# Performance work log

Hardware: AMD Instinct MI355X
Metric: run time of the kernel (lower is better)

The kernel has to match this reference:

```python
import jax, jax.numpy as jnp
import numpy as np

EPS = 1e-5

def setup_inputs() -> dict:
    key = jax.random.key(0)
    k1, k2, k3, k4, k5 = jax.random.split(key, 5)
    N, E, D = 50000, 1600000, 128
    feat = jax.random.normal(k1, (N, D), dtype=jnp.float32)
    edge_index = jax.random.randint(k2, (2, E), 0, N, dtype=jnp.int64)
    W = jax.random.normal(k3, (D, D), dtype=jnp.float32) * (1.0 / np.sqrt(D))
    b = jax.random.normal(k4, (D,), dtype=jnp.float32) * 0.01
    gamma = jnp.ones((D,), dtype=jnp.float32)
    beta = jnp.zeros((D,), dtype=jnp.float32)
    return {"feat": feat, "edge_index": edge_index, "W": W, "b": b, "gamma": gamma, "beta": beta}

def reference(feat, edge_index, W, b, gamma, beta):
    # feat: [N, D] node features; edge_index: [2, E] (src, dst)
    N = feat.shape[0]
    src, dst = edge_index[0], edge_index[1]
    ones = jnp.ones(src.shape, dtype=feat.dtype)
    # out-degree of source nodes, in-degree of destination nodes
    deg_out = jnp.clip(jax.ops.segment_sum(ones, src, num_segments=N), 1.0)
    deg_in = jnp.clip(jax.ops.segment_sum(ones, dst, num_segments=N), 1.0)
    # pre-scale by D_out^{-1/2}, aggregate messages (copy_src + sum)
    feat_src = feat * jax.lax.rsqrt(deg_out)[:, None]        # [N, D]
    agg = jax.ops.segment_sum(feat_src[src], dst, num_segments=N)  # [N, D]
    # linear projection then post-scale by D_in^{-1/2}
    rst = agg @ W.T + b
    rst = rst * jax.lax.rsqrt(deg_in)[:, None]
    # identity residual (in_dim == out_dim)
    rst = rst + feat
    # LayerNorm(out_dim)
    mu = jnp.mean(rst, axis=-1, keepdims=True)
    var = jnp.var(rst, axis=-1, keepdims=True)
    rst = (rst - mu) * jax.lax.rsqrt(var + EPS) * gamma + beta
    # relu activation
    return jax.nn.relu(rst)
```

## Files before the change

kernel.cpp:

```cpp
#include <hip/hip_runtime.h>
#include <hip/hip_fp16.h>

#define LN_EPS 1e-5f
#define D 128
#define TN 16
#define BCAP 768
#define MAXB 4096
#define BBLK 256
#define HBLK 2048
#define NREP 8
#define AGG_LD 136

typedef _Float16 f16x4 __attribute__((ext_vector_type(4)));
typedef float f32x4 __attribute__((ext_vector_type(4)));

__global__ __launch_bounds__(256) void k_build(const int* __restrict__ ei, int E,
        int* __restrict__ cnt_out, int* __restrict__ bcnt,
        unsigned int* __restrict__ bkt, int NB, int Np) {
    __shared__ int h[MAXB];
    __shared__ int cur[MAXB];
    int tid = threadIdx.x;
    int E4 = E >> 2;
    const int4* src4 = (const int4*)ei;
    const int4* dst4 = (const int4*)(ei + E);

    if (blockIdx.x >= BBLK) {
        int* co = cnt_out + (size_t)(blockIdx.x & (NREP - 1)) * Np;
        int gtid = (blockIdx.x - BBLK) * 256 + tid;
        int gstride = (gridDim.x - BBLK) * 256;
        for (int i = gtid; i < E4; i += gstride) {
            int4 s = src4[i];
            atomicAdd(&co[s.x], 1);
            atomicAdd(&co[s.y], 1);
            atomicAdd(&co[s.z], 1);
            atomicAdd(&co[s.w], 1);
        }
        for (int e = (E4 << 2) + gtid; e < E; e += gstride) {
            atomicAdd(&co[ei[e]], 1);
        }
        return;
    }

    int chunk4 = (E4 + BBLK - 1) / BBLK;
    int lo4 = blockIdx.x * chunk4;
    int hi4 = min(E4, lo4 + chunk4);
    bool last = (blockIdx.x == BBLK - 1);

    for (int k = tid; k < NB; k += 256) h[k] = 0;
    __syncthreads();

    for (int i = lo4 + tid; i < hi4; i += 256) {
        int4 d = dst4[i];
        atomicAdd(&h[d.x >> 4], 1);
        atomicAdd(&h[d.y >> 4], 1);
        atomicAdd(&h[d.z >> 4], 1);
        atomicAdd(&h[d.w >> 4], 1);
    }
    if (last) {
        for (int e = (E4 << 2) + tid; e < E; e += 256)
            atomicAdd(&h[ei[E + e] >> 4], 1);
    }
    __syncthreads();

    for (int k = tid; k < NB; k += 256) {
        int c = h[k];
        cur[k] = c ? atomicAdd(&bcnt[k], c) : 0;
    }
    __syncthreads();

    for (int i = lo4 + tid; i < hi4; i += 256) {
        int4 s = src4[i];
        int4 d = dst4[i];
        int p0 = atomicAdd(&cur[d.x >> 4], 1);
        int p1 = atomicAdd(&cur[d.y >> 4], 1);
        int p2 = atomicAdd(&cur[d.z >> 4], 1);
        int p3 = atomicAdd(&cur[d.w >> 4], 1);
        if (p0 < BCAP) bkt[(size_t)(d.x >> 4) * BCAP + p0] = (unsigned)s.x | ((unsigned)(d.x & 15) << 16);
        if (p1 < BCAP) bkt[(size_t)(d.y >> 4) * BCAP + p1] = (unsigned)s.y | ((unsigned)(d.y & 15) << 16);
        if (p2 < BCAP) bkt[(size_t)(d.z >> 4) * BCAP + p2] = (unsigned)s.z | ((unsigned)(d.z & 15) << 16);
        if (p3 < BCAP) bkt[(size_t)(d.w >> 4) * BCAP + p3] = (unsigned)s.w | ((unsigned)(d.w & 15) << 16);
    }
    if (last) {
        for (int e = (E4 << 2) + tid; e < E; e += 256) {
            int s = ei[e], dd = ei[E + e];
            int p = atomicAdd(&cur[dd >> 4], 1);
            if (p < BCAP) bkt[(size_t)(dd >> 4) * BCAP + p] = (unsigned)s | ((unsigned)(dd & 15) << 16);
        }
    }
}

__global__ __launch_bounds__(256) void k_rs(const int* __restrict__ cnt_out,
                                            float* __restrict__ rs_out,
                                            const float* __restrict__ W,
                                            __half2* __restrict__ Wh2, int N, int Np) {
    int i = blockIdx.x * blockDim.x + threadIdx.x;
    if (i < N) {
        int so = 0;
        #pragma unroll
        for (int r = 0; r < NREP; ++r) so += cnt_out[(size_t)r * Np + i];
        rs_out[i] = rsqrtf((float)max(so, 1));
    }
    if (i < D * D / 2) {
        float2 w2 = ((const float2*)W)[i];
        Wh2[i] = __floats2half2_rn(w2.x, w2.y);
    }
}

__global__ __launch_bounds__(256) void k_prep(const float4* __restrict__ feat4,
                                              const float* __restrict__ rs_out,
                                              ushort4* __restrict__ feat_h,
                                              int total ) {
    int stride = gridDim.x * blockDim.x;
    for (int i = blockIdx.x * blockDim.x + threadIdx.x; i < total; i += stride) {
        int n = i >> 5;
        float rs = rs_out[n];
        float4 f = feat4[i];
        __half2 lo = __floats2half2_rn(f.x * rs, f.y * rs);
        __half2 hi = __floats2half2_rn(f.z * rs, f.w * rs);
        ushort4 u;
        u.x = __half_as_ushort(__low2half(lo));
        u.y = __half_as_ushort(__high2half(lo));
        u.z = __half_as_ushort(__low2half(hi));
        u.w = __half_as_ushort(__high2half(hi));
        feat_h[i] = u;
    }
}

__global__ __launch_bounds__(512) void k_fused(
        const int* __restrict__ bcnt, const unsigned int* __restrict__ bkt,
        const uint4* __restrict__ fh16, const _Float16* __restrict__ Wh,
        const float* __restrict__ bias, const float* __restrict__ gamma,
        const float* __restrict__ beta, const float* __restrict__ feat,
        float* __restrict__ out, int N) {
    __shared__ _Float16 aggH[TN * AGG_LD];
    __shared__ float redS[8][TN];
    __shared__ float redQ[8][TN];
    __shared__ unsigned short blist[BCAP];
    __shared__ int bstart[TN + 1];
    __shared__ int bfill[TN];
    __shared__ int bdeg[TN];

    int tid  = threadIdx.x;
    int wv   = tid >> 6;
    int lane = tid & 63;
    int l15  = lane & 15;
    int lg   = lane >> 4;

    int dA = wv * 16 + l15;
    float bd0 = bias[dA];
    float gd0 = gamma[dA];
    float bt0 = beta[dA];

    f16x4 Bf[8];
    #pragma unroll
    for (int kb = 0; kb < 8; ++kb)
        Bf[kb] = *reinterpret_cast<const f16x4*>(&Wh[(size_t)dA * D + kb * 16 + lg * 4]);

    int ntiles = (N + TN - 1) / TN;

    int t = blockIdx.x;
    unsigned v0c = 0, v1c = 0;
    int ec_c = 0;
    if (t < ntiles) {
        ec_c = min(bcnt[t], BCAP);
        v0c = bkt[(size_t)t * BCAP + tid];
        v1c = (tid + 512 < BCAP) ? bkt[(size_t)t * BCAP + tid + 512] : 0u;
    }

    for (; t < ntiles; t += gridDim.x) {
        int t2 = t + gridDim.x;
        unsigned v0n = 0, v1n = 0;
        int ec_n = 0;
        if (t2 < ntiles) {
            ec_n = min(bcnt[t2], BCAP);
            v0n = bkt[(size_t)t2 * BCAP + tid];
            v1n = (tid + 512 < BCAP) ? bkt[(size_t)t2 * BCAP + tid + 512] : 0u;
        }

        int nbase = t * TN;
        __syncthreads();
        if (tid < TN) { bdeg[tid] = 0; bfill[tid] = 0; }
        __syncthreads();

        if (tid < ec_c)       atomicAdd(&bdeg[v0c >> 16], 1);
        if (tid + 512 < ec_c) atomicAdd(&bdeg[v1c >> 16], 1);
        __syncthreads();

        if (tid < 16) {
            int v = bdeg[tid];
            int inc = v;
            #pragma unroll
            for (int off = 1; off < 16; off <<= 1) {
                int u = __shfl_up(inc, off, 16);
                if (tid >= off) inc += u;
            }
            bstart[tid] = inc - v;
            if (tid == 15) bstart[16] = inc;
        }
        __syncthreads();

        if (tid < ec_c) {
            int node = v0c >> 16;
            int slot = bstart[node] + atomicAdd(&bfill[node], 1);
            blist[slot] = (unsigned short)(v0c & 0xFFFF);
        }
        if (tid + 512 < ec_c) {
            int node = v1c >> 16;
            int slot = bstart[node] + atomicAdd(&bfill[node], 1);
            blist[slot] = (unsigned short)(v1c & 0xFFFF);
        }
        __syncthreads();

        {
            int row  = wv * 2 + (lg & 1);
            int half = lg >> 1;
            int n    = nbase + row;
            float va[8];
            #pragma unroll
            for (int k = 0; k < 8; ++k) va[k] = 0.0f;
            if (n < N) {
                int deg = bdeg[row];
                int st  = bstart[row];
                int cnt = (deg > half) ? ((deg - half + 1) >> 1) : 0;
                int base = st + half;
                int j = 0;
                for (; j + 8 <= cnt; j += 8) {
                    int ss[8];
                    #pragma unroll
                    for (int k = 0; k < 8; ++k) ss[k] = blist[base + 2 * (j + k)];
                    uint4 vv[8];
                    #pragma unroll
                    for (int k = 0; k < 8; ++k) vv[k] = fh16[(size_t)ss[k] * 16 + l15];
                    #pragma unroll
                    for (int k = 0; k < 8; ++k) {
                        float2 f;
                        f = __half22float2(__builtin_bit_cast(__half2, vv[k].x));
                        va[0] += f.x; va[1] += f.y;
                        f = __half22float2(__builtin_bit_cast(__half2, vv[k].y));
                        va[2] += f.x; va[3] += f.y;
                        f = __half22float2(__builtin_bit_cast(__half2, vv[k].z));
                        va[4] += f.x; va[5] += f.y;
                        f = __half22float2(__builtin_bit_cast(__half2, vv[k].w));
                        va[6] += f.x; va[7] += f.y;
                    }
                }
                for (; j < cnt; ++j) {
                    int s = blist[base + 2 * j];
                    uint4 vv = fh16[(size_t)s * 16 + l15];
                    float2 f;
                    f = __half22float2(__builtin_bit_cast(__half2, vv.x)); va[0] += f.x; va[1] += f.y;
                    f = __half22float2(__builtin_bit_cast(__half2, vv.y)); va[2] += f.x; va[3] += f.y;
                    f = __half22float2(__builtin_bit_cast(__half2, vv.z)); va[4] += f.x; va[5] += f.y;
                    f = __half22float2(__builtin_bit_cast(__half2, vv.w)); va[6] += f.x; va[7] += f.y;
                }
            }
            #pragma unroll
            for (int k = 0; k < 8; ++k) va[k] += __shfl_xor(va[k], 32);
            if (half == 0) {
                __half2 h0 = __floats2half2_rn(va[0], va[1]);
                __half2 h1 = __floats2half2_rn(va[2], va[3]);
                __half2 h2 = __floats2half2_rn(va[4], va[5]);
                __half2 h3 = __floats2half2_rn(va[6], va[7]);
                uint4 o;
                o.x = __builtin_bit_cast(unsigned int, h0);
                o.y = __builtin_bit_cast(unsigned int, h1);
                o.z = __builtin_bit_cast(unsigned int, h2);
                o.w = __builtin_bit_cast(unsigned int, h3);
                *reinterpret_cast<uint4*>(&aggH[row * AGG_LD + l15 * 8]) = o;
            }
        }
        __syncthreads();

        f32x4 acc = {0.0f, 0.0f, 0.0f, 0.0f};
        #pragma unroll
        for (int kb = 0; kb < 8; ++kb) {
            f16x4 a = *reinterpret_cast<const f16x4*>(&aggH[l15 * AGG_LD + kb * 16 + lg * 4]);
            acc = __builtin_amdgcn_mfma_f32_16x16x16f16(a, Bf[kb], acc, 0, 0, 0);
        }

        float rv[4];
        #pragma unroll
        for (int r = 0; r < 4; ++r) {
            int m = lg * 4 + r;
            int n = nbase + m;
            float f0 = 0.0f;
            if (n < N) {
                float rsin = rsqrtf((float)max(bdeg[m], 1));
                f0 = (acc[r] + bd0) * rsin + feat[(size_t)n * D + dA];
            }
            rv[r] = f0;
            float s = f0;
            float q = f0 * f0;
            s += __shfl_xor(s, 1);  q += __shfl_xor(q, 1);
            s += __shfl_xor(s, 2);  q += __shfl_xor(q, 2);
            s += __shfl_xor(s, 4);  q += __shfl_xor(q, 4);
            s += __shfl_xor(s, 8);  q += __shfl_xor(q, 8);
            if (l15 == 0) { redS[wv][m] = s; redQ[wv][m] = q; }
        }
        __syncthreads();

        #pragma unroll
        for (int r = 0; r < 4; ++r) {
            int m = lg * 4 + r;
            int n = nbase + m;
            if (n < N) {
                float S = redS[0][m] + redS[1][m] + redS[2][m] + redS[3][m]
                        + redS[4][m] + redS[5][m] + redS[6][m] + redS[7][m];
                float Q = redQ[0][m] + redQ[1][m] + redQ[2][m] + redQ[3][m]
                        + redQ[4][m] + redQ[5][m] + redQ[6][m] + redQ[7][m];
                float mu  = S * (1.0f / 128.0f);
                float var = Q * (1.0f / 128.0f) - mu * mu;
                float inv = rsqrtf(var + LN_EPS);
                float v0 = (rv[r] - mu) * inv * gd0 + bt0;
                out[(size_t)n * D + dA] = fmaxf(v0, 0.0f);
            }
        }

        v0c = v0n; v1c = v1n; ec_c = ec_n;
    }
}

extern "C" void kernel_launch(void* const* d_in, const int* in_sizes, int n_in,
                              void* d_out, int out_size, void* d_ws, size_t ws_size,
                              hipStream_t stream) {
    const float* feat  = (const float*)d_in[0];
    const int*   ei    = (const int*)  d_in[1];
    const float* W     = (const float*)d_in[2];
    const float* bias  = (const float*)d_in[3];
    const float* gamma = (const float*)d_in[4];
    const float* beta  = (const float*)d_in[5];
    float* out = (float*)d_out;

    const int N  = in_sizes[0] / D;
    const int E  = in_sizes[1] / 2;
    const int NB = (N + TN - 1) / TN;

    const size_t Np  = ((size_t)N + 1023) & ~(size_t)1023;
    const size_t NBp = ((size_t)NB + 1023) & ~(size_t)1023;
    int*   cnt_out = (int*)d_ws;
    int*   bcnt    = cnt_out + NREP * Np;
    float* rs_out  = (float*)(bcnt + NBp);
    _Float16* Wh   = (_Float16*)(rs_out + Np);
    unsigned int* bkt = (unsigned int*)((int*)(rs_out + Np) + D * D / 2);
    ushort4* feat_h   = (ushort4*)(bkt + (size_t)NB * BCAP);

    hipMemsetAsync(d_ws, 0, (NREP * Np + NBp) * sizeof(int), stream);

    k_build<<<BBLK + HBLK, 256, 0, stream>>>(ei, E, cnt_out, bcnt, bkt, NB, (int)Np);
    int nblk = (max(N, D * D / 2) + 255) / 256;
    k_rs<<<nblk, 256, 0, stream>>>(cnt_out, rs_out, W, (__half2*)Wh, N, (int)Np);
    k_prep<<<2048, 256, 0, stream>>>((const float4*)feat, rs_out, feat_h, N * 32);
    int fgrid = (NB + 1) / 2;
    if (fgrid < 1) fgrid = 1;
    k_fused<<<fgrid, 512, 0, stream>>>(bcnt, bkt,
                                       (const uint4*)feat_h, Wh, bias, gamma,
                                       beta, feat, out, N);
}
```

Baseline: 187.1 us.

## Double node tile to 32 rows and give each row one lane group

Each destination tile grows from 16 to 32 nodes, and the bucket capacity grows to 1536 edges. Bucketing now shifts by 5 and packs a 5-bit local node id. In the fused kernel each 16-lane group gathers all edges of one row on its own, so the cross-half shuffle reduction goes away. Two MFMA accumulators then cover the 32 rows against the same register-resident W fragments, and LayerNorm handles both halves. The aim is to spread per-tile overhead (syncs, prefix scan, bucket loads) over more nodes, at the cost of a longer serial gather per lane group and more registers.

```diff
diff --git a/kernel.cpp b/kernel.cpp
--- a/kernel.cpp
+++ b/kernel.cpp
@@ -3,9 +3,9 @@
 
 #define LN_EPS 1e-5f
 #define D 128
-#define TN 16
-#define BCAP 768
-#define MAXB 4096
+#define TN 32
+#define BCAP 1536
+#define MAXB 2048
 #define BBLK 256
 #define HBLK 2048
 #define NREP 8
@@ -51,14 +51,14 @@
 
     for (int i = lo4 + tid; i < hi4; i += 256) {
         int4 d = dst4[i];
-        atomicAdd(&h[d.x >> 4], 1);
-        atomicAdd(&h[d.y >> 4], 1);
-        atomicAdd(&h[d.z >> 4], 1);
-        atomicAdd(&h[d.w >> 4], 1);
+        atomicAdd(&h[d.x >> 5], 1);
+        atomicAdd(&h[d.y >> 5], 1);
+        atomicAdd(&h[d.z >> 5], 1);
+        atomicAdd(&h[d.w >> 5], 1);
     }
     if (last) {
         for (int e = (E4 << 2) + tid; e < E; e += 256)
-            atomicAdd(&h[ei[E + e] >> 4], 1);
+            atomicAdd(&h[ei[E + e] >> 5], 1);
     }
     __syncthreads();
 
@@ -71,20 +71,20 @@
     for (int i = lo4 + tid; i < hi4; i += 256) {
         int4 s = src4[i];
         int4 d = dst4[i];
-        int p0 = atomicAdd(&cur[d.x >> 4], 1);
-        int p1 = atomicAdd(&cur[d.y >> 4], 1);
-        int p2 = atomicAdd(&cur[d.z >> 4], 1);
-        int p3 = atomicAdd(&cur[d.w >> 4], 1);
-        if (p0 < BCAP) bkt[(size_t)(d.x >> 4) * BCAP + p0] = (unsigned)s.x | ((unsigned)(d.x & 15) << 16);
-        if (p1 < BCAP) bkt[(size_t)(d.y >> 4) * BCAP + p1] = (unsigned)s.y | ((unsigned)(d.y & 15) << 16);
-        if (p2 < BCAP) bkt[(size_t)(d.z >> 4) * BCAP + p2] = (unsigned)s.z | ((unsigned)(d.z & 15) << 16);
-        if (p3 < BCAP) bkt[(size_t)(d.w >> 4) * BCAP + p3] = (unsigned)s.w | ((unsigned)(d.w & 15) << 16);
+        int p0 = atomicAdd(&cur[d.x >> 5], 1);
+        int p1 = atomicAdd(&cur[d.y >> 5], 1);
+        int p2 = atomicAdd(&cur[d.z >> 5], 1);
+        int p3 = atomicAdd(&cur[d.w >> 5], 1);
+        if (p0 < BCAP) bkt[(size_t)(d.x >> 5) * BCAP + p0] = (unsigned)s.x | ((unsigned)(d.x & 31) << 16);
+        if (p1 < BCAP) bkt[(size_t)(d.y >> 5) * BCAP + p1] = (unsigned)s.y | ((unsigned)(d.y & 31) << 16);
+        if (p2 < BCAP) bkt[(size_t)(d.z >> 5) * BCAP + p2] = (unsigned)s.z | ((unsigned)(d.z & 31) << 16);
+        if (p3 < BCAP) bkt[(size_t)(d.w >> 5) * BCAP + p3] = (unsigned)s.w | ((unsigned)(d.w & 31) << 16);
     }
     if (last) {
         for (int e = (E4 << 2) + tid; e < E; e += 256) {
             int s = ei[e], dd = ei[E + e];
-            int p = atomicAdd(&cur[dd >> 4], 1);
-            if (p < BCAP) bkt[(size_t)(dd >> 4) * BCAP + p] = (unsigned)s | ((unsigned)(dd & 15) << 16);
+            int p = atomicAdd(&cur[dd >> 5], 1);
+            if (p < BCAP) bkt[(size_t)(dd >> 5) * BCAP + p] = (unsigned)s | ((unsigned)(dd & 31) << 16);
         }
     }
 }
@@ -159,22 +159,24 @@
     int ntiles = (N + TN - 1) / TN;
 
     int t = blockIdx.x;
-    unsigned v0c = 0, v1c = 0;
+    unsigned v0c = 0, v1c = 0, v2c = 0;
     int ec_c = 0;
     if (t < ntiles) {
         ec_c = min(bcnt[t], BCAP);
         v0c = bkt[(size_t)t * BCAP + tid];
-        v1c = (tid + 512 < BCAP) ? bkt[(size_t)t * BCAP + tid + 512] : 0u;
+        v1c = bkt[(size_t)t * BCAP + tid + 512];
+        v2c = bkt[(size_t)t * BCAP + tid + 1024];
     }
 
     for (; t < ntiles; t += gridDim.x) {
         int t2 = t + gridDim.x;
-        unsigned v0n = 0, v1n = 0;
+        unsigned v0n = 0, v1n = 0, v2n = 0;
         int ec_n = 0;
         if (t2 < ntiles) {
             ec_n = min(bcnt[t2], BCAP);
             v0n = bkt[(size_t)t2 * BCAP + tid];
-            v1n = (tid + 512 < BCAP) ? bkt[(size_t)t2 * BCAP + tid + 512] : 0u;
+            v1n = bkt[(size_t)t2 * BCAP + tid + 512];
+            v2n = bkt[(size_t)t2 * BCAP + tid + 1024];
         }
 
         int nbase = t * TN;
@@ -182,20 +184,21 @@
         if (tid < TN) { bdeg[tid] = 0; bfill[tid] = 0; }
         __syncthreads();
 
-        if (tid < ec_c)       atomicAdd(&bdeg[v0c >> 16], 1);
-        if (tid + 512 < ec_c) atomicAdd(&bdeg[v1c >> 16], 1);
-        __syncthreads();
-
-        if (tid < 16) {
+        if (tid < ec_c)        atomicAdd(&bdeg[v0c >> 16], 1);
+        if (tid + 512 < ec_c)  atomicAdd(&bdeg[v1c >> 16], 1);
+        if (tid + 1024 < ec_c) atomicAdd(&bdeg[v2c >> 16], 1);
+        __syncthreads();
+
+        if (tid < 32) {
             int v = bdeg[tid];
             int inc = v;
             #pragma unroll
-            for (int off = 1; off < 16; off <<= 1) {
-                int u = __shfl_up(inc, off, 16);
+            for (int off = 1; off < 32; off <<= 1) {
+                int u = __shfl_up(inc, off, 32);
                 if (tid >= off) inc += u;
             }
             bstart[tid] = inc - v;
-            if (tid == 15) bstart[16] = inc;
+            if (tid == 31) bstart[32] = inc;
         }
         __syncthreads();
 
@@ -209,25 +212,27 @@
             int slot = bstart[node] + atomicAdd(&bfill[node], 1);
             blist[slot] = (unsigned short)(v1c & 0xFFFF);
         }
+        if (tid + 1024 < ec_c) {
+            int node = v2c >> 16;
+            int slot = bstart[node] + atomicAdd(&bfill[node], 1);
+            blist[slot] = (unsigned short)(v2c & 0xFFFF);
+        }
         __syncthreads();
 
         {
-            int row  = wv * 2 + (lg & 1);
-            int half = lg >> 1;
-            int n    = nbase + row;
+            int row = wv * 4 + lg;
+            int n   = nbase + row;
             float va[8];
             #pragma unroll
             for (int k = 0; k < 8; ++k) va[k] = 0.0f;
             if (n < N) {
                 int deg = bdeg[row];
                 int st  = bstart[row];
-                int cnt = (deg > half) ? ((deg - half + 1) >> 1) : 0;
-                int base = st + half;
                 int j = 0;
-                for (; j + 8 <= cnt; j += 8) {
+                for (; j + 8 <= deg; j += 8) {
                     int ss[8];
                     #pragma unroll
-                    for (int k = 0; k < 8; ++k) ss[k] = blist[base + 2 * (j + k)];
+                    for (int k = 0; k < 8; ++k) ss[k] = blist[st + j + k];
                     uint4 vv[8];
                     #pragma unroll
                     for (int k = 0; k < 8; ++k) vv[k] = fh16[(size_t)ss[k] * 16 + l15];
@@ -244,8 +249,8 @@
                         va[6] += f.x; va[7] += f.y;
                     }
                 }
-                for (; j < cnt; ++j) {
-                    int s = blist[base + 2 * j];
+                for (; j < deg; ++j) {
+                    int s = blist[st + j];
                     uint4 vv = fh16[(size_t)s * 16 + l15];
                     float2 f;
                     f = __half22float2(__builtin_bit_cast(__half2, vv.x)); va[0] += f.x; va[1] += f.y;
@@ -254,69 +259,92 @@
                     f = __half22float2(__builtin_bit_cast(__half2, vv.w)); va[6] += f.x; va[7] += f.y;
                 }
             }
-            #pragma unroll
-            for (int k = 0; k < 8; ++k) va[k] += __shfl_xor(va[k], 32);
-            if (half == 0) {
-                __half2 h0 = __floats2half2_rn(va[0], va[1]);
-                __half2 h1 = __floats2half2_rn(va[2], va[3]);
-                __half2 h2 = __floats2half2_rn(va[4], va[5]);
-                __half2 h3 = __floats2half2_rn(va[6], va[7]);
-                uint4 o;
-                o.x = __builtin_bit_cast(unsigned int, h0);
-                o.y = __builtin_bit_cast(unsigned int, h1);
-                o.z = __builtin_bit_cast(unsigned int, h2);
-                o.w = __builtin_bit_cast(unsigned int, h3);
-                *reinterpret_cast<uint4*>(&aggH[row * AGG_LD + l15 * 8]) = o;
-            }
-        }
-        __syncthreads();
-
-        f32x4 acc = {0.0f, 0.0f, 0.0f, 0.0f};
+            __half2 h0 = __floats2half2_rn(va[0], va[1]);
+            __half2 h1 = __floats2half2_rn(va[2], va[3]);
+            __half2 h2 = __floats2half2_rn(va[4], va[5]);
+            __half2 h3 = __floats2half2_rn(va[6], va[7]);
+            uint4 o;
+            o.x = __builtin_bit_cast(unsigned int, h0);
+            o.y = __builtin_bit_cast(unsigned int, h1);
+            o.z = __builtin_bit_cast(unsigned int, h2);
+            o.w = __builtin_bit_cast(unsigned int, h3);
+            *reinterpret_cast<uint4*>(&aggH[row * AGG_LD + l15 * 8]) = o;
+        }
+        __syncthreads();
+
+        f32x4 acc0 = {0.0f, 0.0f, 0.0f, 0.0f};
+        f32x4 acc1 = {0.0f, 0.0f, 0.0f, 0.0f};
         #pragma unroll
         for (int kb = 0; kb < 8; ++kb) {
-            f16x4 a = *reinterpret_cast<const f16x4*>(&aggH[l15 * AGG_LD + kb * 16 + lg * 4]);
-            acc = __builtin_amdgcn_mfma_f32_16x16x16f16(a, Bf[kb], acc, 0, 0, 0);
-        }
-
-        float rv[4];
+            f16x4 a0 = *reinterpret_cast<const f16x4*>(&aggH[l15 * AGG_LD + kb * 16 + lg * 4]);
+            f16x4 a1 = *reinterpret_cast<const f16x4*>(&aggH[(16 + l15) * AGG_LD + kb * 16 + lg * 4]);
+            acc0 = __builtin_amdgcn_mfma_f32_16x16x16f16(a0, Bf[kb], acc0, 0, 0, 0);
+            acc1 = __builtin_amdgcn_mfma_f32_16x16x16f16(a1, Bf[kb], acc1, 0, 0, 0);
+        }
+
+        float rv0[4], rv1[4];
         #pragma unroll
         for (int r = 0; r < 4; ++r) {
-            int m = lg * 4 + r;
-            int n = nbase + m;
-            float f0 = 0.0f;
-            if (n < N) {
-                float rsin = rsqrtf((float)max(bdeg[m], 1));
-                f0 = (acc[r] + bd0) * rsin + feat[(size_t)n * D + dA];
-            }
-            rv[r] = f0;
-            float s = f0;
-            float q = f0 * f0;
-            s += __shfl_xor(s, 1);  q += __shfl_xor(q, 1);
-            s += __shfl_xor(s, 2);  q += __shfl_xor(q, 2);
-            s += __shfl_xor(s, 4);  q += __shfl_xor(q, 4);
-            s += __shfl_xor(s, 8);  q += __shfl_xor(q, 8);
-            if (l15 == 0) { redS[wv][m] = s; redQ[wv][m] = q; }
+            int m0 = lg * 4 + r;
+            int m1 = 16 + m0;
+            int n0 = nbase + m0;
+            int n1 = nbase + m1;
+            float f0 = 0.0f, f1 = 0.0f;
+            if (n0 < N) {
+                float rsin = rsqrtf((float)max(bdeg[m0], 1));
+                f0 = (acc0[r] + bd0) * rsin + feat[(size_t)n0 * D + dA];
+            }
+            if (n1 < N) {
+                float rsin = rsqrtf((float)max(bdeg[m1], 1));
+                f1 = (acc1[r] + bd0) * rsin + feat[(size_t)n1 * D + dA];
+            }
+            rv0[r] = f0; rv1[r] = f1;
+            float s0 = f0, q0 = f0 * f0;
+            float s1 = f1, q1 = f1 * f1;
+            s0 += __shfl_xor(s0, 1);  q0 += __shfl_xor(q0, 1);
+            s0 += __shfl_xor(s0, 2);  q0 += __shfl_xor(q0, 2);
+            s0 += __shfl_xor(s0, 4);  q0 += __shfl_xor(q0, 4);
+            s0 += __shfl_xor(s0, 8);  q0 += __shfl_xor(q0, 8);
+            s1 += __shfl_xor(s1, 1);  q1 += __shfl_xor(q1, 1);
+            s1 += __shfl_xor(s1, 2);  q1 += __shfl_xor(q1, 2);
+            s1 += __shfl_xor(s1, 4);  q1 += __shfl_xor(q1, 4);
+            s1 += __shfl_xor(s1, 8);  q1 += __shfl_xor(q1, 8);
+            if (l15 == 0) {
+                redS[wv][m0] = s0; redQ[wv][m0] = q0;
+                redS[wv][m1] = s1; redQ[wv][m1] = q1;
+            }
         }
         __syncthreads();
 
         #pragma unroll
         for (int r = 0; r < 4; ++r) {
-            int m = lg * 4 + r;
-            int n = nbase + m;
-            if (n < N) {
-                float S = redS[0][m] + redS[1][m] + redS[2][m] + redS[3][m]
-                        + redS[4][m] + redS[5][m] + redS[6][m] + redS[7][m];
-                float Q = redQ[0][m] + redQ[1][m] + redQ[2][m] + redQ[3][m]
-                        + redQ[4][m] + redQ[5][m] + redQ[6][m] + redQ[7][m];
+            int m0 = lg * 4 + r;
+            int m1 = 16 + m0;
+            int n0 = nbase + m0;
+            int n1 = nbase + m1;
+            if (n0 < N) {
+                float S = redS[0][m0] + redS[1][m0] + redS[2][m0] + redS[3][m0]
+                        + redS[4][m0] + redS[5][m0] + redS[6][m0] + redS[7][m0];
+                float Q = redQ[0][m0] + redQ[1][m0] + redQ[2][m0] + redQ[3][m0]
+                        + redQ[4][m0] + redQ[5][m0] + redQ[6][m0] + redQ[7][m0];
                 float mu  = S * (1.0f / 128.0f);
                 float var = Q * (1.0f / 128.0f) - mu * mu;
                 float inv = rsqrtf(var + LN_EPS);
-                float v0 = (rv[r] - mu) * inv * gd0 + bt0;
-                out[(size_t)n * D + dA] = fmaxf(v0, 0.0f);
-            }
-        }
-
-        v0c = v0n; v1c = v1n; ec_c = ec_n;
+                out[(size_t)n0 * D + dA] = fmaxf((rv0[r] - mu) * inv * gd0 + bt0, 0.0f);
+            }
+            if (n1 < N) {
+                float S = redS[0][m1] + redS[1][m1] + redS[2][m1] + redS[3][m1]
+                        + redS[4][m1] + redS[5][m1] + redS[6][m1] + redS[7][m1];
+                float Q = redQ[0][m1] + redQ[1][m1] + redQ[2][m1] + redQ[3][m1]
+                        + redQ[4][m1] + redQ[5][m1] + redQ[6][m1] + redQ[7][m1];
+                float mu  = S * (1.0f / 128.0f);
+                float var = Q * (1.0f / 128.0f) - mu * mu;
+                float inv = rsqrtf(var + LN_EPS);
+                out[(size_t)n1 * D + dA] = fmaxf((rv1[r] - mu) * inv * gd0 + bt0, 0.0f);
+            }
+        }
+
+        v0c = v0n; v1c = v1n; v2c = v2n; ec_c = ec_n;
     }
 }
 
```

Result: slower. 212.4 us (+13.5%).
